# Performance work log

Hardware: AMD Instinct MI355X
Metric: run time of the kernel (lower is better)

## Reference

```python
import jax, jax.numpy as jnp
import numpy as np

N = 100000   # nodes
H = 128      # hidden_size
T = 32       # transitivity_size
MD = 16      # mask_dim
K = 3        # propagation steps
E_S = 600000 # spatial edges
E_D = 600000 # dom edges


def setup_inputs() -> dict:
    key = jax.random.key(0)
    ks = jax.random.split(key, 12)
    return {
        "x": jax.random.normal(ks[0], (N, H), jnp.float32),
        "mask": jax.random.uniform(ks[1], (N, MD), jnp.float32),
        "spatial_edge_index": jax.random.randint(ks[2], (2, E_S), 0, N, jnp.int64 if jax.config.jax_enable_x64 else jnp.int32),
        "dom_edge_index": jax.random.randint(ks[3], (2, E_D), 0, N, jnp.int64 if jax.config.jax_enable_x64 else jnp.int32),
        "spatial_edge_attr": jax.random.normal(ks[4], (E_S, 4), jnp.float32),
        "dom_edge_attr": jax.random.normal(ks[5], (E_D, 1), jnp.float32),
        "W_trans": jax.random.normal(ks[6], (2 * H, T), jnp.float32) / np.sqrt(2 * H),
        "b_trans": jnp.zeros((T,), jnp.float32),
        "W_pos": jax.random.normal(ks[7], (4 + T, 1), jnp.float32) / np.sqrt(4 + T),
        "b_pos": jnp.zeros((1,), jnp.float32),
        "W_dom": jax.random.normal(ks[8], (1 + T, 1), jnp.float32) / np.sqrt(1 + T),
        "b_dom": jnp.zeros((1,), jnp.float32),
    }


def _edge_attrs(x, edge_index, W, b):
    # EdgeAttrs: gather src/dst node features, concat, linear + tanh -> [E, T]
    h = jnp.concatenate([x[edge_index[0]], x[edge_index[1]]], axis=1)
    return jnp.tanh(h @ W + b)


def _edge_mask(edge_attr, mask, edge_index, W, b, k_steps, n_nodes):
    # EdgeMask: per-edge gating weight in (0,1), then K rounds of
    # gate-weighted max-propagation of the node mask along edges.
    ew = jax.nn.sigmoid(edge_attr @ W + b)  # [E, 1]
    src, dst = edge_index[0], edge_index[1]
    m = mask
    for _ in range(k_steps):
        msg = m[src] * ew                                  # [E, MD]
        agg = jax.ops.segment_max(msg, dst, num_segments=n_nodes)
        m = jnp.maximum(m, agg)                            # -inf (empty segs) absorbed
    return m, ew


def reference(x, mask, spatial_edge_index, dom_edge_index, spatial_edge_attr,
              dom_edge_attr, W_trans, b_trans, W_pos, b_pos, W_dom, b_dom):
    n_nodes = x.shape[0]
    # spatial branch (projection is dom -> no safe_bc_edges broadcast)
    trans_s = _edge_attrs(x, spatial_edge_index, W_trans, b_trans)
    pos_in = jnp.concatenate([spatial_edge_attr, trans_s], axis=1)  # [E_S, 4+T]
    pos_mask, _pos_ew = _edge_mask(pos_in, mask, spatial_edge_index, W_pos, b_pos, K, n_nodes)
    # dom branch
    trans_d = _edge_attrs(x, dom_edge_index, W_trans, b_trans)
    dom_in = jnp.concatenate([dom_edge_attr, trans_d], axis=1)      # [E_D, 1+T]
    dom_mask, _dom_ew = _edge_mask(dom_in, mask, dom_edge_index, W_dom, b_dom, K, n_nodes)
    return jnp.maximum(mask, jnp.maximum(pos_mask, dom_mask))
```

## Files before the change

### kernel.cpp

```cpp
#include <hip/hip_runtime.h>
#include <hip/hip_bf16.h>
#include <stdint.h>

#define NNODES 100000
#define HID 128
#define TSZ 32
#define MDIM 16
#define ES 600000
#define ED 600000
#define ETOT (ES + ED)
#define GN (2 * NNODES)
#define GNP 200704
#define SCAN_BLOCKS 196
#define NP8 (NNODES * 8)
#define GN8 (GN * 8)
#define PQ_BLOCKS 1563
#define CNT_BLK 586

typedef unsigned short ushort_t;

__device__ __forceinline__ float bflo(unsigned u) { return __uint_as_float(u << 16); }
__device__ __forceinline__ float bfhi(unsigned u) { return __uint_as_float(u & 0xffff0000u); }

__device__ __forceinline__ unsigned f2bf(float f) {
    unsigned u = __float_as_uint(f);
    return (u + 0x7FFFu + ((u >> 16) & 1u)) >> 16;
}
__device__ __forceinline__ unsigned packbf(float lo, float hi) {
    return f2bf(lo) | (f2bf(hi) << 16);
}

__device__ __forceinline__ float tanh_fast(float v) {
    float z = __expf(2.f * v);
    return 1.f - 2.f / (z + 1.f);
}

__global__ __launch_bounds__(256) void k_pq(const float* __restrict__ x,
                                            const float* __restrict__ Wt,
                                            const float* __restrict__ bt,
                                            char* __restrict__ pq) {
    __shared__ float xs[64][132];
    __shared__ float wl[64][130];
    const int tid = threadIdx.x;
    const int n0 = blockIdx.x * 64;

    for (int i = tid; i < 4096; i += 256) {
        int h = i >> 5, c = i & 31;
        float a = Wt[i];
        float b = Wt[4096 + i];
        wl[c][h] = a;
        wl[c + 32][h] = b;
    }
    const float4* xsrc = (const float4*)(x + (size_t)n0 * 128);
#pragma unroll
    for (int i = 0; i < 8; ++i) {
        int idx = tid + 256 * i;
        int node = idx >> 5;
        int rem = idx & 31;
        if (n0 + node < NNODES) {
            float4 v = xsrc[idx];
            *(float4*)&xs[node][rem * 4] = v;
        }
    }
    __syncthreads();

    const int l = tid & 63;
    const int w = tid >> 6;
    const int c0 = l & 15;
    const int ng = w * 16 + (l >> 4) * 4;
    float acc[4][4] = {};
#pragma unroll 4
    for (int h = 0; h < 128; h += 2) {
        float2 xv[4], wv[4];
#pragma unroll
        for (int m = 0; m < 4; ++m) xv[m] = *(const float2*)&xs[ng + m][h];
#pragma unroll
        for (int m = 0; m < 4; ++m) wv[m] = *(const float2*)&wl[c0 + 16 * m][h];
#pragma unroll
        for (int a = 0; a < 4; ++a)
#pragma unroll
            for (int b = 0; b < 4; ++b)
                acc[a][b] = fmaf(xv[a].y, wv[b].y, fmaf(xv[a].x, wv[b].x, acc[a][b]));
    }
    float bv[4];
#pragma unroll
    for (int b = 0; b < 4; ++b) {
        int c = c0 + 16 * b;
        bv[b] = (c < 32) ? bt[c] : 0.f;
    }
    __syncthreads();
    char* buf = (char*)&xs[0][0];
#pragma unroll
    for (int a = 0; a < 4; ++a) {
#pragma unroll
        for (int b = 0; b < 4; ++b) {
            float v = acc[a][b] + bv[b];
            int q = __float2int_rn(v * 32.f);
            q = max(-127, min(127, q));
            buf[(ng + a) * 64 + c0 + 16 * b] = (char)q;
        }
    }
    __syncthreads();
    uint4 v4 = ((const uint4*)buf)[tid];
    ((uint4*)(pq + (size_t)blockIdx.x * 4096))[tid] = v4;
}

__global__ __launch_bounds__(256) void k_initcount(const float* __restrict__ mask,
                                                   unsigned* __restrict__ m_a,
                                                   const int* __restrict__ sdst,
                                                   const int* __restrict__ ddst,
                                                   int* __restrict__ counts) {
    const int tid = threadIdx.x;
    int b = (int)blockIdx.x;
    if (b < 3125) {
        int idx = b * 256 + tid;
        float2 v = ((const float2*)mask)[idx];
        unsigned p = packbf(v.x, v.y);
        m_a[idx] = p;
        m_a[NP8 + idx] = p;
        return;
    }
    b -= 3125;
    const int* dst;
    int add;
    if (b < CNT_BLK) { dst = sdst; add = 0; }
    else { b -= CNT_BLK; dst = ddst; add = NNODES; }
    int e0 = (b * 256 + tid) * 4;
    if (e0 + 4 <= 600000) {
        int4 d = *(const int4*)(dst + e0);
        atomicAdd(&counts[d.x + add], 1);
        atomicAdd(&counts[d.y + add], 1);
        atomicAdd(&counts[d.z + add], 1);
        atomicAdd(&counts[d.w + add], 1);
    } else {
        for (int e = e0; e < 600000; ++e) atomicAdd(&counts[dst[e] + add], 1);
    }
}

__global__ __launch_bounds__(256) void k_scanfused(const int* __restrict__ counts,
                                                   int* __restrict__ bsum,
                                                   int* __restrict__ flag,
                                                   int* __restrict__ off,
                                                   int* __restrict__ cursor) {
    __shared__ int sh[256];
    const int tid = threadIdx.x;
    const int bid = (int)blockIdx.x;
    int4 v = ((const int4*)counts)[bid * 256 + tid];
    int tot = v.x + v.y + v.z + v.w;
    sh[tid] = tot;
    __syncthreads();
    for (int o = 1; o < 256; o <<= 1) {
        int add = (tid >= o) ? sh[tid - o] : 0;
        __syncthreads();
        sh[tid] += add;
        __syncthreads();
    }
    int incl = sh[tid];
    if (tid == 255) bsum[bid] = incl;
    if (tid == 0) {
        __threadfence();
        atomicAdd(flag, 1);
        while (__hip_atomic_load(flag, __ATOMIC_RELAXED, __HIP_MEMORY_SCOPE_AGENT) < SCAN_BLOCKS) {}
        __threadfence();
    }
    __syncthreads();
    sh[tid] = (tid < SCAN_BLOCKS) ? bsum[tid] : 0;
    __syncthreads();
    for (int o = 1; o < 256; o <<= 1) {
        int add = (tid >= o) ? sh[tid - o] : 0;
        __syncthreads();
        sh[tid] += add;
        __syncthreads();
    }
    int base = (bid > 0) ? sh[bid - 1] : 0;
    int excl = base + incl - tot;
    int4 o4;
    o4.x = excl;
    o4.y = o4.x + v.x;
    o4.z = o4.y + v.y;
    o4.w = o4.z + v.z;
    ((int4*)off)[bid * 256 + tid] = o4;
    ((int4*)cursor)[bid * 256 + tid] = o4;
}

__global__ void k_ewfill(const char* __restrict__ pq,
                         const int* __restrict__ ssrc, const int* __restrict__ sdst,
                         const int* __restrict__ dsrc, const int* __restrict__ ddst,
                         const float* __restrict__ sattr, const float* __restrict__ dattr,
                         const float* __restrict__ Wp, const float* __restrict__ bp,
                         const float* __restrict__ Wd, const float* __restrict__ bd,
                         int* __restrict__ cursor, unsigned* __restrict__ csr) {
    int e = blockIdx.x * 256 + threadIdx.x;
    if (e >= ETOT) return;
    int src, dst, dstg, srcg;
    float acc;
    const float* wt;
    if (e < ES) {
        src = ssrc[e];
        dst = sdst[e];
        dstg = dst;
        srcg = src;
        const float4 a = *(const float4*)(sattr + (size_t)e * 4);
        acc = bp[0] + a.x * Wp[0] + a.y * Wp[1] + a.z * Wp[2] + a.w * Wp[3];
        wt = Wp + 4;
    } else {
        int ed = e - ES;
        src = dsrc[ed];
        dst = ddst[ed];
        dstg = dst + NNODES;
        srcg = src + NNODES;
        acc = bd[0] + dattr[ed] * Wd[0];
        wt = Wd + 1;
    }
    const uint4* Pp = (const uint4*)(pq + (size_t)src * 64);
    const uint4* Qp = (const uint4*)(pq + (size_t)dst * 64 + 32);
    uint4 pa = Pp[0], pb = Pp[1];
    uint4 qa = Qp[0], qb = Qp[1];
    unsigned pw[8] = {pa.x, pa.y, pa.z, pa.w, pb.x, pb.y, pb.z, pb.w};
    unsigned qw[8] = {qa.x, qa.y, qa.z, qa.w, qb.x, qb.y, qb.z, qb.w};
#pragma unroll
    for (int d = 0; d < 8; ++d) {
        unsigned a = pw[d], b = qw[d];
#pragma unroll
        for (int k = 0; k < 4; ++k) {
            int pi = (int)(char)(a >> (8 * k));
            int qi = (int)(char)(b >> (8 * k));
            float t = tanh_fast((float)(pi + qi) * 0.03125f);
            acc = fmaf(t, wt[d * 4 + k], acc);
        }
    }
    float ew = 1.f / (1.f + __expf(-acc));
    unsigned entry = ((unsigned)srcg << 14) | (unsigned)(ew * 16383.f + 0.5f);
    int pos = atomicAdd(&cursor[dstg], 1);
    csr[pos] = entry;
}

template <int TAG>
__global__ __launch_bounds__(256) void k_round_t(const unsigned* __restrict__ m_in,
                                                 unsigned* __restrict__ m_out,
                                                 const int* __restrict__ off,
                                                 const unsigned* __restrict__ csr) {
    int idx = blockIdx.x * 256 + threadIdx.x;
    if (idx >= 2 * GN) return;
    int g = idx >> 1;
    int jp = (idx & 1) * 4;
    int p0 = off[g], p1 = off[g + 1];
    uint4 cur = *(const uint4*)&m_in[g * 8 + jp];
    float v0l = bflo(cur.x), v0h = bfhi(cur.x);
    float v1l = bflo(cur.y), v1h = bfhi(cur.y);
    float v2l = bflo(cur.z), v2h = bfhi(cur.z);
    float v3l = bflo(cur.w), v3h = bfhi(cur.w);
    int p = p0;
    for (; p + 1 < p1; p += 2) {
        unsigned e0 = csr[p], e1 = csr[p + 1];
        uint4 s0 = *(const uint4*)&m_in[(e0 >> 14) * 8 + jp];
        uint4 s1 = *(const uint4*)&m_in[(e1 >> 14) * 8 + jp];
        float w0 = (float)(e0 & 16383u) * (1.f / 16383.f);
        float w1 = (float)(e1 & 16383u) * (1.f / 16383.f);
        v0l = fmaxf(v0l, fmaxf(bflo(s0.x) * w0, bflo(s1.x) * w1));
        v0h = fmaxf(v0h, fmaxf(bfhi(s0.x) * w0, bfhi(s1.x) * w1));
        v1l = fmaxf(v1l, fmaxf(bflo(s0.y) * w0, bflo(s1.y) * w1));
        v1h = fmaxf(v1h, fmaxf(bfhi(s0.y) * w0, bfhi(s1.y) * w1));
        v2l = fmaxf(v2l, fmaxf(bflo(s0.z) * w0, bflo(s1.z) * w1));
        v2h = fmaxf(v2h, fmaxf(bfhi(s0.z) * w0, bfhi(s1.z) * w1));
        v3l = fmaxf(v3l, fmaxf(bflo(s0.w) * w0, bflo(s1.w) * w1));
        v3h = fmaxf(v3h, fmaxf(bfhi(s0.w) * w0, bfhi(s1.w) * w1));
    }
    if (p < p1) {
        unsigned e0 = csr[p];
        uint4 s0 = *(const uint4*)&m_in[(e0 >> 14) * 8 + jp];
        float w0 = (float)(e0 & 16383u) * (1.f / 16383.f);
        v0l = fmaxf(v0l, bflo(s0.x) * w0);
        v0h = fmaxf(v0h, bfhi(s0.x) * w0);
        v1l = fmaxf(v1l, bflo(s0.y) * w0);
        v1h = fmaxf(v1h, bfhi(s0.y) * w0);
        v2l = fmaxf(v2l, bflo(s0.z) * w0);
        v2h = fmaxf(v2h, bfhi(s0.z) * w0);
        v3l = fmaxf(v3l, bflo(s0.w) * w0);
        v3h = fmaxf(v3h, bfhi(s0.w) * w0);
    }
    uint4 o4;
    o4.x = packbf(v0l, v0h);
    o4.y = packbf(v1l, v1h);
    o4.z = packbf(v2l, v2h);
    o4.w = packbf(v3l, v3h);
    *(uint4*)&m_out[g * 8 + jp] = o4;
}

__global__ __launch_bounds__(256) void k_round_final(const unsigned* __restrict__ m_in,
                                                     float* __restrict__ out,
                                                     const int* __restrict__ off,
                                                     const unsigned* __restrict__ csr) {
    int idx = blockIdx.x * 256 + threadIdx.x;
    if (idx >= 2 * NNODES) return;
    int g = idx >> 1;
    int jp = (idx & 1) * 4;
    uint4 c0 = *(const uint4*)&m_in[g * 8 + jp];
    uint4 c1 = *(const uint4*)&m_in[(g + NNODES) * 8 + jp];
    float v0l = fmaxf(bflo(c0.x), bflo(c1.x)), v0h = fmaxf(bfhi(c0.x), bfhi(c1.x));
    float v1l = fmaxf(bflo(c0.y), bflo(c1.y)), v1h = fmaxf(bfhi(c0.y), bfhi(c1.y));
    float v2l = fmaxf(bflo(c0.z), bflo(c1.z)), v2h = fmaxf(bfhi(c0.z), bfhi(c1.z));
    float v3l = fmaxf(bflo(c0.w), bflo(c1.w)), v3h = fmaxf(bfhi(c0.w), bfhi(c1.w));
#pragma unroll
    for (int br = 0; br < 2; ++br) {
        int gg = g + br * NNODES;
        int p0 = off[gg], p1 = off[gg + 1];
        for (int p = p0; p < p1; ++p) {
            unsigned e0 = csr[p];
            uint4 s0 = *(const uint4*)&m_in[(e0 >> 14) * 8 + jp];
            float w0 = (float)(e0 & 16383u) * (1.f / 16383.f);
            v0l = fmaxf(v0l, bflo(s0.x) * w0);
            v0h = fmaxf(v0h, bfhi(s0.x) * w0);
            v1l = fmaxf(v1l, bflo(s0.y) * w0);
            v1h = fmaxf(v1h, bfhi(s0.y) * w0);
            v2l = fmaxf(v2l, bflo(s0.z) * w0);
            v2h = fmaxf(v2h, bfhi(s0.z) * w0);
            v3l = fmaxf(v3l, bflo(s0.w) * w0);
            v3h = fmaxf(v3h, bfhi(s0.w) * w0);
        }
    }
    float* op = out + (size_t)g * 16 + jp * 2;
    *(float4*)op = make_float4(v0l, v0h, v1l, v1h);
    *(float4*)(op + 4) = make_float4(v2l, v2h, v3l, v3h);
}

extern "C" void kernel_launch(void* const* d_in, const int* in_sizes, int n_in,
                              void* d_out, int out_size, void* d_ws, size_t ws_size,
                              hipStream_t stream) {
    const float* x     = (const float*)d_in[0];
    const float* mask  = (const float*)d_in[1];
    const int*   sei   = (const int*)d_in[2];
    const int*   dei   = (const int*)d_in[3];
    const float* sattr = (const float*)d_in[4];
    const float* dattr = (const float*)d_in[5];
    const float* Wt    = (const float*)d_in[6];
    const float* bt    = (const float*)d_in[7];
    const float* Wp    = (const float*)d_in[8];
    const float* bp    = (const float*)d_in[9];
    const float* Wd    = (const float*)d_in[10];
    const float* bd    = (const float*)d_in[11];
    float* out = (float*)d_out;

    char* ws = (char*)d_ws;
    size_t o = 0;
    auto take = [&](size_t bytes) -> char* {
        char* p = ws + o;
        o = (o + bytes + 255) & ~(size_t)255;
        return p;
    };
    char* pq      = take((size_t)PQ_BLOCKS * 4096);
    int* counts   = (int*)take((size_t)GNP * 4 + 256);
    int* flag     = counts + GNP;
    int* off      = (int*)take((size_t)GNP * 4);
    int* cursor   = (int*)take((size_t)GNP * 4);
    int* bsum     = (int*)take(256 * 4);
    unsigned* csr = (unsigned*)take((size_t)ETOT * 4);
    unsigned* m_a = (unsigned*)take((size_t)GN8 * 4);
    unsigned* m_b = (unsigned*)take((size_t)GN8 * 4);

    hipMemsetAsync(counts, 0, (size_t)GNP * 4 + 256, stream);
    k_pq<<<PQ_BLOCKS, 256, 0, stream>>>(x, Wt, bt, pq);
    k_initcount<<<3125 + 2 * CNT_BLK, 256, 0, stream>>>(mask, m_a, sei + ES, dei + ED, counts);
    k_scanfused<<<SCAN_BLOCKS, 256, 0, stream>>>(counts, bsum, flag, off, cursor);
    k_ewfill<<<(ETOT + 255) / 256, 256, 0, stream>>>(pq,
        sei, sei + ES, dei, dei + ED, sattr, dattr, Wp, bp, Wd, bd, cursor, csr);
    k_round_t<0><<<(2 * GN + 255) / 256, 256, 0, stream>>>(m_a, m_b, off, csr);
    k_round_t<1><<<(2 * GN + 255) / 256, 256, 0, stream>>>(m_b, m_a, off, csr);
    k_round_final<<<(2 * NNODES + 255) / 256, 256, 0, stream>>>(m_a, out, off, csr);
}
```

Baseline: 343.9 us.

## Fuse three propagation rounds into one persistent kernel with grid barriers

Replaces the three separate propagation launches with one persistent kernel of 1024 blocks that grid-strides over the work and uses atomic-counter grid barriers between rounds. The aim is to remove kernel launch gaps and tail effects between the dependent rounds. In exchange, each round runs with fewer resident threads than a full-grid launch, and the spin-wait barriers add overhead. The barriers assume all 1024 blocks are co-resident and could deadlock if they are not.

```diff
diff --git a/kernel.cpp b/kernel.cpp
--- a/kernel.cpp
+++ b/kernel.cpp
@@ -16,6 +16,7 @@
 #define GN8 (GN * 8)
 #define PQ_BLOCKS 1563
 #define CNT_BLK 586
+#define PROP_NB 1024
 
 typedef unsigned short ushort_t;
 
@@ -235,13 +236,11 @@
     csr[pos] = entry;
 }
 
-template <int TAG>
-__global__ __launch_bounds__(256) void k_round_t(const unsigned* __restrict__ m_in,
-                                                 unsigned* __restrict__ m_out,
-                                                 const int* __restrict__ off,
-                                                 const unsigned* __restrict__ csr) {
-    int idx = blockIdx.x * 256 + threadIdx.x;
-    if (idx >= 2 * GN) return;
+__device__ __forceinline__ void prop_half(const unsigned* __restrict__ m_in,
+                                          unsigned* __restrict__ m_out,
+                                          const int* __restrict__ off,
+                                          const unsigned* __restrict__ csr,
+                                          int idx) {
     int g = idx >> 1;
     int jp = (idx & 1) * 4;
     int p0 = off[g], p1 = off[g + 1];
@@ -287,41 +286,60 @@
     *(uint4*)&m_out[g * 8 + jp] = o4;
 }
 
-__global__ __launch_bounds__(256) void k_round_final(const unsigned* __restrict__ m_in,
-                                                     float* __restrict__ out,
-                                                     const int* __restrict__ off,
-                                                     const unsigned* __restrict__ csr) {
-    int idx = blockIdx.x * 256 + threadIdx.x;
-    if (idx >= 2 * NNODES) return;
-    int g = idx >> 1;
-    int jp = (idx & 1) * 4;
-    uint4 c0 = *(const uint4*)&m_in[g * 8 + jp];
-    uint4 c1 = *(const uint4*)&m_in[(g + NNODES) * 8 + jp];
-    float v0l = fmaxf(bflo(c0.x), bflo(c1.x)), v0h = fmaxf(bfhi(c0.x), bfhi(c1.x));
-    float v1l = fmaxf(bflo(c0.y), bflo(c1.y)), v1h = fmaxf(bfhi(c0.y), bfhi(c1.y));
-    float v2l = fmaxf(bflo(c0.z), bflo(c1.z)), v2h = fmaxf(bfhi(c0.z), bfhi(c1.z));
-    float v3l = fmaxf(bflo(c0.w), bflo(c1.w)), v3h = fmaxf(bfhi(c0.w), bfhi(c1.w));
-#pragma unroll
-    for (int br = 0; br < 2; ++br) {
-        int gg = g + br * NNODES;
-        int p0 = off[gg], p1 = off[gg + 1];
-        for (int p = p0; p < p1; ++p) {
-            unsigned e0 = csr[p];
-            uint4 s0 = *(const uint4*)&m_in[(e0 >> 14) * 8 + jp];
-            float w0 = (float)(e0 & 16383u) * (1.f / 16383.f);
-            v0l = fmaxf(v0l, bflo(s0.x) * w0);
-            v0h = fmaxf(v0h, bfhi(s0.x) * w0);
-            v1l = fmaxf(v1l, bflo(s0.y) * w0);
-            v1h = fmaxf(v1h, bfhi(s0.y) * w0);
-            v2l = fmaxf(v2l, bflo(s0.z) * w0);
-            v2h = fmaxf(v2h, bfhi(s0.z) * w0);
-            v3l = fmaxf(v3l, bflo(s0.w) * w0);
-            v3h = fmaxf(v3h, bfhi(s0.w) * w0);
+__device__ __forceinline__ void grid_bar(int* flag) {
+    __syncthreads();
+    if (threadIdx.x == 0) {
+        __threadfence();
+        atomicAdd(flag, 1);
+        while (__hip_atomic_load(flag, __ATOMIC_RELAXED, __HIP_MEMORY_SCOPE_AGENT) < PROP_NB) {}
+        __threadfence();
+    }
+    __syncthreads();
+}
+
+__global__ __launch_bounds__(256, 4) void k_prop(unsigned* __restrict__ m_a,
+                                                 unsigned* __restrict__ m_b,
+                                                 const int* __restrict__ off,
+                                                 const unsigned* __restrict__ csr,
+                                                 int* __restrict__ flags,
+                                                 float* __restrict__ out) {
+    const int t0 = (int)blockIdx.x * 256 + threadIdx.x;
+    const int STRIDE = PROP_NB * 256;
+    for (int idx = t0; idx < 2 * GN; idx += STRIDE) prop_half(m_a, m_b, off, csr, idx);
+    grid_bar(&flags[0]);
+    for (int idx = t0; idx < 2 * GN; idx += STRIDE) prop_half(m_b, m_a, off, csr, idx);
+    grid_bar(&flags[1]);
+    for (int idx = t0; idx < 2 * NNODES; idx += STRIDE) {
+        int g = idx >> 1;
+        int jp = (idx & 1) * 4;
+        uint4 c0 = *(const uint4*)&m_a[g * 8 + jp];
+        uint4 c1 = *(const uint4*)&m_a[(g + NNODES) * 8 + jp];
+        float v0l = fmaxf(bflo(c0.x), bflo(c1.x)), v0h = fmaxf(bfhi(c0.x), bfhi(c1.x));
+        float v1l = fmaxf(bflo(c0.y), bflo(c1.y)), v1h = fmaxf(bfhi(c0.y), bfhi(c1.y));
+        float v2l = fmaxf(bflo(c0.z), bflo(c1.z)), v2h = fmaxf(bfhi(c0.z), bfhi(c1.z));
+        float v3l = fmaxf(bflo(c0.w), bflo(c1.w)), v3h = fmaxf(bfhi(c0.w), bfhi(c1.w));
+#pragma unroll
+        for (int br = 0; br < 2; ++br) {
+            int gg = g + br * NNODES;
+            int p0 = off[gg], p1 = off[gg + 1];
+            for (int p = p0; p < p1; ++p) {
+                unsigned e0 = csr[p];
+                uint4 s0 = *(const uint4*)&m_a[(e0 >> 14) * 8 + jp];
+                float w0 = (float)(e0 & 16383u) * (1.f / 16383.f);
+                v0l = fmaxf(v0l, bflo(s0.x) * w0);
+                v0h = fmaxf(v0h, bfhi(s0.x) * w0);
+                v1l = fmaxf(v1l, bflo(s0.y) * w0);
+                v1h = fmaxf(v1h, bfhi(s0.y) * w0);
+                v2l = fmaxf(v2l, bflo(s0.z) * w0);
+                v2h = fmaxf(v2h, bfhi(s0.z) * w0);
+                v3l = fmaxf(v3l, bflo(s0.w) * w0);
+                v3h = fmaxf(v3h, bfhi(s0.w) * w0);
+            }
         }
-    }
-    float* op = out + (size_t)g * 16 + jp * 2;
-    *(float4*)op = make_float4(v0l, v0h, v1l, v1h);
-    *(float4*)(op + 4) = make_float4(v2l, v2h, v3l, v3h);
+        float* op = out + (size_t)g * 16 + jp * 2;
+        *(float4*)op = make_float4(v0l, v0h, v1l, v1h);
+        *(float4*)(op + 4) = make_float4(v2l, v2h, v3l, v3h);
+    }
 }
 
 extern "C" void kernel_launch(void* const* d_in, const int* in_sizes, int n_in,
@@ -350,7 +368,8 @@
     };
     char* pq      = take((size_t)PQ_BLOCKS * 4096);
     int* counts   = (int*)take((size_t)GNP * 4 + 256);
-    int* flag     = counts + GNP;
+    int* scanflag = counts + GNP;
+    int* propflags = counts + GNP + 1;
     int* off      = (int*)take((size_t)GNP * 4);
     int* cursor   = (int*)take((size_t)GNP * 4);
     int* bsum     = (int*)take(256 * 4);
@@ -361,10 +380,8 @@
     hipMemsetAsync(counts, 0, (size_t)GNP * 4 + 256, stream);
     k_pq<<<PQ_BLOCKS, 256, 0, stream>>>(x, Wt, bt, pq);
     k_initcount<<<3125 + 2 * CNT_BLK, 256, 0, stream>>>(mask, m_a, sei + ES, dei + ED, counts);
-    k_scanfused<<<SCAN_BLOCKS, 256, 0, stream>>>(counts, bsum, flag, off, cursor);
+    k_scanfused<<<SCAN_BLOCKS, 256, 0, stream>>>(counts, bsum, scanflag, off, cursor);
     k_ewfill<<<(ETOT + 255) / 256, 256, 0, stream>>>(pq,
         sei, sei + ES, dei, dei + ED, sattr, dattr, Wp, bp, Wd, bd, cursor, csr);
-    k_round_t<0><<<(2 * GN + 255) / 256, 256, 0, stream>>>(m_a, m_b, off, csr);
-    k_round_t<1><<<(2 * GN + 255) / 256, 256, 0, stream>>>(m_b, m_a, off, csr);
-    k_round_final<<<(2 * NNODES + 255) / 256, 256, 0, stream>>>(m_a, out, off, csr);
-}
+    k_prop<<<PROP_NB, 256, 0, stream>>>(m_a, m_b, off, csr, propflags, out);
+}
```

Result: slower. 616.3 us (+79.2%).

## Merge projection and init/count kernels; split fused scan into three kernels

Applied to the files above, without the earlier changes.

The x@W_trans projection kernel and the mask-init/degree-count kernel become one launch, with the work chosen by block index, so the two independent jobs can overlap on the GPU. The single-pass scan that used a global spin-wait flag is replaced by a three-kernel reduce, scan-prefix and scan-apply sequence. This drops the spin barrier, which relies on every block being resident at once, but adds two kernel launches. The merged kernel now reserves the projection kernel's large shared-memory footprint for the lightweight init/count blocks as well, which can lower their occupancy.

```diff
diff --git a/kernel.cpp b/kernel.cpp
--- a/kernel.cpp
+++ b/kernel.cpp
@@ -35,83 +35,84 @@
     return 1.f - 2.f / (z + 1.f);
 }
 
-__global__ __launch_bounds__(256) void k_pq(const float* __restrict__ x,
-                                            const float* __restrict__ Wt,
-                                            const float* __restrict__ bt,
-                                            char* __restrict__ pq) {
+__global__ __launch_bounds__(256) void k_prep(const float* __restrict__ x,
+                                              const float* __restrict__ Wt,
+                                              const float* __restrict__ bt,
+                                              char* __restrict__ pq,
+                                              const float* __restrict__ mask,
+                                              unsigned* __restrict__ m_a,
+                                              const int* __restrict__ sdst,
+                                              const int* __restrict__ ddst,
+                                              int* __restrict__ counts) {
     __shared__ float xs[64][132];
     __shared__ float wl[64][130];
     const int tid = threadIdx.x;
-    const int n0 = blockIdx.x * 64;
-
-    for (int i = tid; i < 4096; i += 256) {
-        int h = i >> 5, c = i & 31;
-        float a = Wt[i];
-        float b = Wt[4096 + i];
-        wl[c][h] = a;
-        wl[c + 32][h] = b;
-    }
-    const float4* xsrc = (const float4*)(x + (size_t)n0 * 128);
-#pragma unroll
-    for (int i = 0; i < 8; ++i) {
-        int idx = tid + 256 * i;
-        int node = idx >> 5;
-        int rem = idx & 31;
-        if (n0 + node < NNODES) {
-            float4 v = xsrc[idx];
-            *(float4*)&xs[node][rem * 4] = v;
-        }
-    }
-    __syncthreads();
-
-    const int l = tid & 63;
-    const int w = tid >> 6;
-    const int c0 = l & 15;
-    const int ng = w * 16 + (l >> 4) * 4;
-    float acc[4][4] = {};
+    int b = (int)blockIdx.x;
+
+    if (b < PQ_BLOCKS) {
+        const int n0 = b * 64;
+        for (int i = tid; i < 4096; i += 256) {
+            int h = i >> 5, c = i & 31;
+            float a = Wt[i];
+            float bv2 = Wt[4096 + i];
+            wl[c][h] = a;
+            wl[c + 32][h] = bv2;
+        }
+        const float4* xsrc = (const float4*)(x + (size_t)n0 * 128);
+#pragma unroll
+        for (int i = 0; i < 8; ++i) {
+            int idx = tid + 256 * i;
+            int node = idx >> 5;
+            int rem = idx & 31;
+            if (n0 + node < NNODES) {
+                float4 v = xsrc[idx];
+                *(float4*)&xs[node][rem * 4] = v;
+            }
+        }
+        __syncthreads();
+
+        const int l = tid & 63;
+        const int w = tid >> 6;
+        const int c0 = l & 15;
+        const int ng = w * 16 + (l >> 4) * 4;
+        float acc[4][4] = {};
 #pragma unroll 4
-    for (int h = 0; h < 128; h += 2) {
-        float2 xv[4], wv[4];
-#pragma unroll
-        for (int m = 0; m < 4; ++m) xv[m] = *(const float2*)&xs[ng + m][h];
-#pragma unroll
-        for (int m = 0; m < 4; ++m) wv[m] = *(const float2*)&wl[c0 + 16 * m][h];
-#pragma unroll
-        for (int a = 0; a < 4; ++a)
-#pragma unroll
-            for (int b = 0; b < 4; ++b)
-                acc[a][b] = fmaf(xv[a].y, wv[b].y, fmaf(xv[a].x, wv[b].x, acc[a][b]));
-    }
-    float bv[4];
-#pragma unroll
-    for (int b = 0; b < 4; ++b) {
-        int c = c0 + 16 * b;
-        bv[b] = (c < 32) ? bt[c] : 0.f;
-    }
-    __syncthreads();
-    char* buf = (char*)&xs[0][0];
-#pragma unroll
-    for (int a = 0; a < 4; ++a) {
-#pragma unroll
-        for (int b = 0; b < 4; ++b) {
-            float v = acc[a][b] + bv[b];
-            int q = __float2int_rn(v * 32.f);
-            q = max(-127, min(127, q));
-            buf[(ng + a) * 64 + c0 + 16 * b] = (char)q;
-        }
-    }
-    __syncthreads();
-    uint4 v4 = ((const uint4*)buf)[tid];
-    ((uint4*)(pq + (size_t)blockIdx.x * 4096))[tid] = v4;
-}
-
-__global__ __launch_bounds__(256) void k_initcount(const float* __restrict__ mask,
-                                                   unsigned* __restrict__ m_a,
-                                                   const int* __restrict__ sdst,
-                                                   const int* __restrict__ ddst,
-                                                   int* __restrict__ counts) {
-    const int tid = threadIdx.x;
-    int b = (int)blockIdx.x;
+        for (int h = 0; h < 128; h += 2) {
+            float2 xv[4], wv[4];
+#pragma unroll
+            for (int m = 0; m < 4; ++m) xv[m] = *(const float2*)&xs[ng + m][h];
+#pragma unroll
+            for (int m = 0; m < 4; ++m) wv[m] = *(const float2*)&wl[c0 + 16 * m][h];
+#pragma unroll
+            for (int a = 0; a < 4; ++a)
+#pragma unroll
+                for (int c = 0; c < 4; ++c)
+                    acc[a][c] = fmaf(xv[a].y, wv[c].y, fmaf(xv[a].x, wv[c].x, acc[a][c]));
+        }
+        float bv[4];
+#pragma unroll
+        for (int c = 0; c < 4; ++c) {
+            int cc = c0 + 16 * c;
+            bv[c] = (cc < 32) ? bt[cc] : 0.f;
+        }
+        __syncthreads();
+        char* buf = (char*)&xs[0][0];
+#pragma unroll
+        for (int a = 0; a < 4; ++a) {
+#pragma unroll
+            for (int c = 0; c < 4; ++c) {
+                float v = acc[a][c] + bv[c];
+                int q = __float2int_rn(v * 32.f);
+                q = max(-127, min(127, q));
+                buf[(ng + a) * 64 + c0 + 16 * c] = (char)q;
+            }
+        }
+        __syncthreads();
+        uint4 v4 = ((const uint4*)buf)[tid];
+        ((uint4*)(pq + (size_t)b * 4096))[tid] = v4;
+        return;
+    }
+    b -= PQ_BLOCKS;
     if (b < 3125) {
         int idx = b * 256 + tid;
         float2 v = ((const float2*)mask)[idx];
@@ -137,15 +138,43 @@
     }
 }
 
-__global__ __launch_bounds__(256) void k_scanfused(const int* __restrict__ counts,
-                                                   int* __restrict__ bsum,
-                                                   int* __restrict__ flag,
-                                                   int* __restrict__ off,
-                                                   int* __restrict__ cursor) {
+__global__ __launch_bounds__(256) void k_scan1(const int* __restrict__ counts,
+                                               int* __restrict__ bsum) {
     __shared__ int sh[256];
-    const int tid = threadIdx.x;
-    const int bid = (int)blockIdx.x;
-    int4 v = ((const int4*)counts)[bid * 256 + tid];
+    int tid = threadIdx.x;
+    int4 v = ((const int4*)counts)[blockIdx.x * 256 + tid];
+    sh[tid] = v.x + v.y + v.z + v.w;
+    __syncthreads();
+    for (int o = 128; o > 0; o >>= 1) {
+        if (tid < o) sh[tid] += sh[tid + o];
+        __syncthreads();
+    }
+    if (tid == 0) bsum[blockIdx.x] = sh[0];
+}
+
+__global__ __launch_bounds__(256) void k_scan2(const int* __restrict__ bsum,
+                                               int* __restrict__ prefix) {
+    __shared__ int sh[256];
+    int tid = threadIdx.x;
+    int v = (tid < SCAN_BLOCKS) ? bsum[tid] : 0;
+    sh[tid] = v;
+    __syncthreads();
+    for (int o = 1; o < 256; o <<= 1) {
+        int add = (tid >= o) ? sh[tid - o] : 0;
+        __syncthreads();
+        sh[tid] += add;
+        __syncthreads();
+    }
+    prefix[tid] = sh[tid] - v;
+}
+
+__global__ __launch_bounds__(256) void k_scan3(const int* __restrict__ counts,
+                                               const int* __restrict__ prefix,
+                                               int* __restrict__ off,
+                                               int* __restrict__ cursor) {
+    __shared__ int sh[256];
+    int tid = threadIdx.x;
+    int4 v = ((const int4*)counts)[blockIdx.x * 256 + tid];
     int tot = v.x + v.y + v.z + v.w;
     sh[tid] = tot;
     __syncthreads();
@@ -155,32 +184,14 @@
         sh[tid] += add;
         __syncthreads();
     }
-    int incl = sh[tid];
-    if (tid == 255) bsum[bid] = incl;
-    if (tid == 0) {
-        __threadfence();
-        atomicAdd(flag, 1);
-        while (__hip_atomic_load(flag, __ATOMIC_RELAXED, __HIP_MEMORY_SCOPE_AGENT) < SCAN_BLOCKS) {}
-        __threadfence();
-    }
-    __syncthreads();
-    sh[tid] = (tid < SCAN_BLOCKS) ? bsum[tid] : 0;
-    __syncthreads();
-    for (int o = 1; o < 256; o <<= 1) {
-        int add = (tid >= o) ? sh[tid - o] : 0;
-        __syncthreads();
-        sh[tid] += add;
-        __syncthreads();
-    }
-    int base = (bid > 0) ? sh[bid - 1] : 0;
-    int excl = base + incl - tot;
+    int excl = sh[tid] - tot + prefix[blockIdx.x];
     int4 o4;
     o4.x = excl;
     o4.y = o4.x + v.x;
     o4.z = o4.y + v.y;
     o4.w = o4.z + v.z;
-    ((int4*)off)[bid * 256 + tid] = o4;
-    ((int4*)cursor)[bid * 256 + tid] = o4;
+    ((int4*)off)[blockIdx.x * 256 + tid] = o4;
+    ((int4*)cursor)[blockIdx.x * 256 + tid] = o4;
 }
 
 __global__ void k_ewfill(const char* __restrict__ pq,
@@ -349,19 +360,21 @@
         return p;
     };
     char* pq      = take((size_t)PQ_BLOCKS * 4096);
-    int* counts   = (int*)take((size_t)GNP * 4 + 256);
-    int* flag     = counts + GNP;
+    int* counts   = (int*)take((size_t)GNP * 4);
     int* off      = (int*)take((size_t)GNP * 4);
     int* cursor   = (int*)take((size_t)GNP * 4);
     int* bsum     = (int*)take(256 * 4);
+    int* prefix   = (int*)take(256 * 4);
     unsigned* csr = (unsigned*)take((size_t)ETOT * 4);
     unsigned* m_a = (unsigned*)take((size_t)GN8 * 4);
     unsigned* m_b = (unsigned*)take((size_t)GN8 * 4);
 
-    hipMemsetAsync(counts, 0, (size_t)GNP * 4 + 256, stream);
-    k_pq<<<PQ_BLOCKS, 256, 0, stream>>>(x, Wt, bt, pq);
-    k_initcount<<<3125 + 2 * CNT_BLK, 256, 0, stream>>>(mask, m_a, sei + ES, dei + ED, counts);
-    k_scanfused<<<SCAN_BLOCKS, 256, 0, stream>>>(counts, bsum, flag, off, cursor);
+    hipMemsetAsync(counts, 0, (size_t)GNP * 4, stream);
+    k_prep<<<PQ_BLOCKS + 3125 + 2 * CNT_BLK, 256, 0, stream>>>(
+        x, Wt, bt, pq, mask, m_a, sei + ES, dei + ED, counts);
+    k_scan1<<<SCAN_BLOCKS, 256, 0, stream>>>(counts, bsum);
+    k_scan2<<<1, 256, 0, stream>>>(bsum, prefix);
+    k_scan3<<<SCAN_BLOCKS, 256, 0, stream>>>(counts, prefix, off, cursor);
     k_ewfill<<<(ETOT + 255) / 256, 256, 0, stream>>>(pq,
         sei, sei + ES, dei, dei + ED, sattr, dattr, Wp, bp, Wd, bd, cursor, csr);
     k_round_t<0><<<(2 * GN + 255) / 256, 256, 0, stream>>>(m_a, m_b, off, csr);
```

New measurement: 324.5 us. 5.6% less time.
